# Performance work log

Measured on AMD Instinct MI355X. Metric: run time of the kernel, lower is better.

Reference implementation:

```python
import jax, jax.numpy as jnp
import numpy as np

B, S, D = 128, 200, 1024
QK = D // 8            # qk_dim_div = 8
E = 2 * D              # expand_factor = 2
RESIDUAL_DEPTH = 384.0 # repo global at model_scale=1.0
NUM_BLOCKS = 8.0
LN_EPS = 1e-5


def setup_inputs() -> dict:
    key = jax.random.key(0)
    k0, k1, k2 = jax.random.split(key, 3)
    x = jax.random.normal(k0, (B, S, D), jnp.float32)
    expand_w = (0.5 / np.sqrt(RESIDUAL_DEPTH) / 2.0) * jax.random.normal(k1, (2 * QK + 2 * E, D), jnp.float32)
    project_w = (1.0 / np.sqrt(RESIDUAL_DEPTH) / 2.0 / NUM_BLOCKS) * jax.random.normal(k2, (D, E), jnp.float32)
    ln_gamma = jnp.ones((D,), jnp.float32)
    ln_beta = jnp.zeros((D,), jnp.float32)
    position_bias_mult = jnp.asarray(1.0, jnp.float32)
    return dict(x=x, expand_w=expand_w, project_w=project_w,
                ln_gamma=ln_gamma, ln_beta=ln_beta,
                position_bias_mult=position_bias_mult)


def reference(x, expand_w, project_w, ln_gamma, ln_beta, position_bias_mult):
    _, s, d = x.shape
    qk = d // 8
    e = 2 * d
    v_dim = d

    # LayerNorm (biased variance, eps=1e-5, affine)
    mu = jnp.mean(x, axis=-1, keepdims=True)
    var = jnp.var(x, axis=-1, keepdims=True)
    xn = (x - mu) * jax.lax.rsqrt(var + LN_EPS) * ln_gamma + ln_beta

    # fused expand GEMM (dropout in eval mode = identity)
    h = jnp.einsum('bsd,ed->bse', xn, expand_w)  # [B,S,2qk+2e]
    q = h[..., :qk]
    k = h[..., qk:2 * qk]
    lin = h[..., 2 * qk:2 * qk + e]
    pre = h[..., 2 * qk + e:]

    # GEGLU: linear * exact-erf gelu
    geglu = lin * jax.nn.gelu(pre, approximate=False)
    geglu_local = geglu[..., :e - v_dim]      # [B,S,e-d]
    geglu_value = geglu[..., e - v_dim:]      # [B,S,d]

    # ALiBi-style additive causal bias: softplus(mult)*(j-i) where j<=i, -inf elsewhere
    idx = jnp.arange(s)
    causal = idx[None, :] <= idx[:, None]
    rel = (idx[None, :] - idx[:, None]).astype(x.dtype)  # j - i (<=0 on causal part)
    bias = jnp.where(causal, jax.nn.softplus(position_bias_mult) * rel,
                     jnp.asarray(-jnp.inf, x.dtype))

    # single-head SDPA, scale = 1/sqrt(qk_dim)
    scale = 1.0 / np.sqrt(qk)
    scores = jnp.einsum('bqd,bkd->bqk', q, k) * scale + bias
    attn = jax.nn.softmax(scores, axis=-1)
    att_out = jnp.einsum('bqk,bkv->bqv', attn, geglu_value)  # [B,S,d]

    out = jnp.einsum('bse,de->bsd', jnp.concatenate([geglu_local, att_out], axis=-1), project_w)
    return x + out
```

## Files before the change

kernel.cpp:

```cpp
#include <hip/hip_runtime.h>

#define B_ 128
#define S_ 200
#define D_ 1024
#define QK_ 128
#define E_ 2048
#define HE_ 4352
#define M_ (B_*S_)
#define MPAD_ (M_+32)

typedef unsigned short u16;
typedef __attribute__((ext_vector_type(8))) short bf16x8;
typedef __attribute__((ext_vector_type(4))) float fx4;
typedef __attribute__((ext_vector_type(4))) u16  usx4;

__device__ __forceinline__ u16 f2bf(float f) {
  union { float f; unsigned u; } v; v.f = f;
  unsigned r = v.u + 0x7fffu + ((v.u >> 16) & 1u);
  return (u16)(r >> 16);
}
__device__ __forceinline__ float bf2f(u16 u) {
  union { unsigned u; float f; } v; v.u = ((unsigned)u) << 16;
  return v.f;
}

__global__ __launch_bounds__(256)
void castw_kernel(const float* __restrict__ ew, const float* __restrict__ pw,
                  u16* __restrict__ ewb, u16* __restrict__ pwb) {
  const int n1 = HE_*D_/4, n2 = D_*E_/4;
  const int stride = gridDim.x * blockDim.x;
  for (int i = blockIdx.x*blockDim.x + threadIdx.x; i < n1; i += stride) {
    fx4 v = ((const fx4*)ew)[i];
    usx4 o; o[0]=f2bf(v[0]); o[1]=f2bf(v[1]); o[2]=f2bf(v[2]); o[3]=f2bf(v[3]);
    ((usx4*)ewb)[i] = o;
  }
  for (int i = blockIdx.x*blockDim.x + threadIdx.x; i < n2; i += stride) {
    fx4 v = ((const fx4*)pw)[i];
    usx4 o; o[0]=f2bf(v[0]); o[1]=f2bf(v[1]); o[2]=f2bf(v[2]); o[3]=f2bf(v[3]);
    ((usx4*)pwb)[i] = o;
  }
}

__global__ __launch_bounds__(256)
void ln_kernel(const float* __restrict__ x, const float* __restrict__ gam,
               const float* __restrict__ bet, u16* __restrict__ xn) {
  const int m = blockIdx.x, t = threadIdx.x;
  const fx4 v = *(const fx4*)(x + (size_t)m*D_ + t*4);
  float s  = v[0]+v[1]+v[2]+v[3];
  float s2 = v[0]*v[0]+v[1]*v[1]+v[2]*v[2]+v[3]*v[3];
  #pragma unroll
  for (int off = 32; off; off >>= 1) { s += __shfl_down(s, off); s2 += __shfl_down(s2, off); }
  __shared__ float red[8];
  const int l = t & 63, w = t >> 6;
  if (l == 0) { red[w] = s; red[4+w] = s2; }
  __syncthreads();
  s  = red[0]+red[1]+red[2]+red[3];
  s2 = red[4]+red[5]+red[6]+red[7];
  const float mu  = s * (1.f/D_);
  const float var = s2 * (1.f/D_) - mu*mu;
  const float rs  = rsqrtf(var + 1e-5f);
  const fx4 g4 = *(const fx4*)(gam + t*4);
  const fx4 b4 = *(const fx4*)(bet + t*4);
  usx4 o;
  #pragma unroll
  for (int j = 0; j < 4; ++j) o[j] = f2bf((v[j]-mu)*rs*g4[j] + b4[j]);
  *(usx4*)(xn + (size_t)m*D_ + t*4) = o;
}

template<int EPI>
__global__ __launch_bounds__(256)
void gemm_bt(const u16* __restrict__ A, const u16* __restrict__ Bt,
             void* __restrict__ Cp, const float* __restrict__ resid,
             int K, int ldc, int gx) {
  const int nwg = gridDim.x;
  const int q8 = nwg >> 3;
  const int swz = (blockIdx.x & 7) * q8 + (blockIdx.x >> 3);
  const int m0 = (swz / gx) * 128, n0 = (swz % gx) * 128;
  __shared__ __align__(16) u16 As[128*32];
  __shared__ __align__(16) u16 Bs[128*32];
  const int t = threadIdx.x, l = t & 63, w = t >> 6;
  const int wr = w >> 1, wc = w & 1;
  fx4 acc[4][4] = {};
  const int srow = l >> 2, scol = (l & 3) * 8;
  const u16* agp = A  + (size_t)(m0 + w*16 + srow)*K + scol;
  const u16* bgp = Bt + (size_t)(n0 + w*16 + srow)*K + scol;
  for (int k0 = 0; k0 < K; k0 += 32) {
    #pragma unroll
    for (int i = 0; i < 2; ++i) {
      __builtin_amdgcn_global_load_lds(
        (const __attribute__((address_space(1))) unsigned int*)(agp + (size_t)i*64*K + k0),
        (__attribute__((address_space(3))) unsigned int*)(As + (w*16 + i*64)*32), 16, 0, 0);
      __builtin_amdgcn_global_load_lds(
        (const __attribute__((address_space(1))) unsigned int*)(bgp + (size_t)i*64*K + k0),
        (__attribute__((address_space(3))) unsigned int*)(Bs + (w*16 + i*64)*32), 16, 0, 0);
    }
    __syncthreads();
    bf16x8 af[4], bfv[4];
    const u16* ap = As + (wr*64 + (l & 15))*32 + (l >> 4)*8;
    const u16* bp = Bs + (wc*64 + (l & 15))*32 + (l >> 4)*8;
    #pragma unroll
    for (int i = 0; i < 4; ++i) {
      af[i]  = *(const bf16x8*)(ap + i*16*32);
      bfv[i] = *(const bf16x8*)(bp + i*16*32);
    }
    #pragma unroll
    for (int mi = 0; mi < 4; ++mi)
      #pragma unroll
      for (int ni = 0; ni < 4; ++ni)
        acc[mi][ni] = __builtin_amdgcn_mfma_f32_16x16x32_bf16(af[mi], bfv[ni], acc[mi][ni], 0, 0, 0);
    __syncthreads();
  }
  const int rb = (l >> 4)*4, cb = l & 15;
  #pragma unroll
  for (int mi = 0; mi < 4; ++mi)
    #pragma unroll
    for (int ni = 0; ni < 4; ++ni) {
      const int col = n0 + wc*64 + ni*16 + cb;
      #pragma unroll
      for (int r = 0; r < 4; ++r) {
        const int row = m0 + wr*64 + mi*16 + rb + r;
        const size_t idx = (size_t)row*ldc + col;
        if (EPI == 0) ((u16*)Cp)[idx] = f2bf(acc[mi][ni][r]);
        else          ((float*)Cp)[idx] = acc[mi][ni][r] + resid[idx];
      }
    }
}

__global__ __launch_bounds__(256)
void fused_expand(const u16* __restrict__ A, const u16* __restrict__ Bt,
                  u16* __restrict__ A2, float* __restrict__ Vv) {
  const int nwg = gridDim.x;
  const int q8 = nwg >> 3;
  const int swz = (blockIdx.x & 7) * q8 + (blockIdx.x >> 3);
  const int m0 = (swz >> 4) * 128;
  const int n0e = (swz & 15) * 128;
  __shared__ __align__(16) u16 As[128*32];
  __shared__ __align__(16) u16 Bs[128*32];
  const int t = threadIdx.x, l = t & 63, w = t >> 6;
  const int wr = w >> 1, wc = w & 1;
  const int srow = l >> 2, scol = (l & 3) * 8;
  const u16* agp = A + (size_t)(m0 + w*16 + srow)*D_ + scol;
  const u16* bgp_pre = Bt + (size_t)(2*QK_ + E_ + n0e + w*16 + srow)*D_ + scol;
  const u16* bgp_lin = Bt + (size_t)(2*QK_ + n0e + w*16 + srow)*D_ + scol;
  fx4 acc[4][4];
  unsigned gp[4][4][2];
  #pragma unroll
  for (int pass = 0; pass < 2; ++pass) {
    const u16* bgp = pass ? bgp_lin : bgp_pre;
    #pragma unroll
    for (int mi = 0; mi < 4; ++mi)
      #pragma unroll
      for (int ni = 0; ni < 4; ++ni) acc[mi][ni] = (fx4){0.f,0.f,0.f,0.f};
    for (int k0 = 0; k0 < D_; k0 += 32) {
      #pragma unroll
      for (int i = 0; i < 2; ++i) {
        __builtin_amdgcn_global_load_lds(
          (const __attribute__((address_space(1))) unsigned int*)(agp + (size_t)i*64*D_ + k0),
          (__attribute__((address_space(3))) unsigned int*)(As + (w*16 + i*64)*32), 16, 0, 0);
        __builtin_amdgcn_global_load_lds(
          (const __attribute__((address_space(1))) unsigned int*)(bgp + (size_t)i*64*D_ + k0),
          (__attribute__((address_space(3))) unsigned int*)(Bs + (w*16 + i*64)*32), 16, 0, 0);
      }
      __syncthreads();
      bf16x8 af[4], bfv[4];
      const u16* ap = As + (wr*64 + (l & 15))*32 + (l >> 4)*8;
      const u16* bp = Bs + (wc*64 + (l & 15))*32 + (l >> 4)*8;
      #pragma unroll
      for (int i = 0; i < 4; ++i) {
        af[i]  = *(const bf16x8*)(ap + i*16*32);
        bfv[i] = *(const bf16x8*)(bp + i*16*32);
      }
      #pragma unroll
      for (int mi = 0; mi < 4; ++mi)
        #pragma unroll
        for (int ni = 0; ni < 4; ++ni)
          acc[mi][ni] = __builtin_amdgcn_mfma_f32_16x16x32_bf16(af[mi], bfv[ni], acc[mi][ni], 0, 0, 0);
      __syncthreads();
    }
    if (pass == 0) {
      #pragma unroll
      for (int mi = 0; mi < 4; ++mi)
        #pragma unroll
        for (int ni = 0; ni < 4; ++ni)
          #pragma unroll
          for (int h = 0; h < 2; ++h) {
            float p0 = acc[mi][ni][2*h],   g0 = 0.5f*p0*(1.f + erff(p0*0.70710678f));
            float p1 = acc[mi][ni][2*h+1], g1 = 0.5f*p1*(1.f + erff(p1*0.70710678f));
            gp[mi][ni][h] = (unsigned)f2bf(g0) | ((unsigned)f2bf(g1) << 16);
          }
    }
  }
  const int rb = (l >> 4)*4, cb = l & 15;
  #pragma unroll
  for (int mi = 0; mi < 4; ++mi)
    #pragma unroll
    for (int ni = 0; ni < 4; ++ni) {
      const int colc = wc*64 + ni*16 + cb;
      #pragma unroll
      for (int r = 0; r < 4; ++r) {
        const int row = m0 + wr*64 + mi*16 + rb + r;
        const float gv = bf2f((u16)(gp[mi][ni][r>>1] >> ((r&1)*16)));
        const float v = acc[mi][ni][r] * gv;
        if (n0e < D_) A2[(size_t)row*E_ + n0e + colc] = f2bf(v);
        else          Vv[(size_t)row*D_ + (n0e - D_) + colc] = v;
      }
    }
}

__global__ __launch_bounds__(256)
void attn_kernel(const u16* __restrict__ QKb, const float* __restrict__ Vv,
                 const float* __restrict__ pbm, u16* __restrict__ A2) {
  const int b = blockIdx.y, qt = blockIdx.x;
  const int qbase = qt*32;
  const int kmax = (S_ < qbase+32) ? S_ : qbase+32;
  const int nkt = (kmax + 15) >> 4;
  const int t = threadIdx.x, l = t & 63, w = t >> 6;
  __shared__ float ScT[208][40];
  float sp; { float p = pbm[0]; sp = (p > 20.f) ? p : log1pf(__expf(p)); }
  const float scale = 0.08838834764831845f;

  const int ntiles = 2*nkt;
  for (int tile = w; tile < ntiles; tile += 4) {
    const int qt16 = tile & 1, kt16 = tile >> 1;
    const int q0 = qbase + qt16*16, k0 = kt16*16;
    if (k0 > q0 + 15) continue;
    fx4 acc = {0.f, 0.f, 0.f, 0.f};
    const u16* qp = QKb + (size_t)(b*S_ + q0 + (l & 15))*256 + (l >> 4)*8;
    const u16* kp = QKb + (size_t)(b*S_ + k0 + (l & 15))*256 + QK_ + (l >> 4)*8;
    #pragma unroll
    for (int ks = 0; ks < 4; ++ks) {
      bf16x8 a  = *(const bf16x8*)(qp + ks*32);
      bf16x8 bb = *(const bf16x8*)(kp + ks*32);
      acc = __builtin_amdgcn_mfma_f32_16x16x32_bf16(a, bb, acc, 0, 0, 0);
    }
    const int kcol = k0 + (l & 15);
    #pragma unroll
    for (int r = 0; r < 4; ++r) {
      const int qg = q0 + (l >> 4)*4 + r;
      float s = acc[r]*scale + sp*(float)(kcol - qg);
      if (kcol > qg || qg >= S_ || kcol >= S_) s = -1e30f;
      ScT[kcol][qt16*16 + (l >> 4)*4 + r] = s;
    }
  }
  __syncthreads();
  {
    const int r = t >> 3, j = t & 7;
    const int qg = qbase + r;
    if (qg < S_) {
      float mx = -1e30f;
      for (int k = j; k <= qg; k += 8) mx = fmaxf(mx, ScT[k][r]);
      #pragma unroll
      for (int msk = 1; msk < 8; msk <<= 1) mx = fmaxf(mx, __shfl_xor(mx, msk));
      float sum = 0.f;
      for (int k = j; k <= qg; k += 8) { float p = __expf(ScT[k][r] - mx); ScT[k][r] = p; sum += p; }
      #pragma unroll
      for (int msk = 1; msk < 8; msk <<= 1) sum += __shfl_xor(sum, msk);
      const float inv = 1.f / sum;
      for (int k = j; k <= qg; k += 8) ScT[k][r] *= inv;
      for (int k = qg+1+j; k < kmax; k += 8) ScT[k][r] = 0.f;
    }
  }
  __syncthreads();
  fx4 acc[32];
  #pragma unroll
  for (int i = 0; i < 32; ++i) acc[i] = (fx4){0.f,0.f,0.f,0.f};
  const float* vb = Vv + (size_t)b*S_*D_ + w*256 + l*4;
  for (int k = 0; k < kmax; ++k) {
    const fx4 v4 = *(const fx4*)(vb + (size_t)k*D_);
    #pragma unroll
    for (int g = 0; g < 8; ++g) {
      const fx4 p4 = *(const fx4*)&ScT[k][g*4];
      #pragma unroll
      for (int j = 0; j < 4; ++j) acc[g*4+j] += v4 * p4[j];
    }
  }
  #pragma unroll
  for (int qi = 0; qi < 32; ++qi) {
    const int qg = qbase + qi;
    if (qg < S_) {
      usx4 o;
      #pragma unroll
      for (int j = 0; j < 4; ++j) o[j] = f2bf(acc[qi][j]);
      *(usx4*)(A2 + (size_t)(b*S_ + qg)*E_ + D_ + w*256 + l*4) = o;
    }
  }
}

extern "C" void kernel_launch(void* const* d_in, const int* in_sizes, int n_in,
                              void* d_out, int out_size, void* d_ws, size_t ws_size,
                              hipStream_t stream) {
  (void)in_sizes; (void)n_in; (void)out_size; (void)ws_size;
  const float* x   = (const float*)d_in[0];
  const float* ew  = (const float*)d_in[1];
  const float* pw  = (const float*)d_in[2];
  const float* gam = (const float*)d_in[3];
  const float* bet = (const float*)d_in[4];
  const float* pbm = (const float*)d_in[5];
  float* out = (float*)d_out;

  char* ws = (char*)d_ws;
  size_t off = 0;
  auto alloc = [&](size_t bytes) -> void* {
    void* p = ws + off; off += (bytes + 255) & ~(size_t)255; return p;
  };
  u16* xn  = (u16*)alloc((size_t)M_   * D_  * 2);
  u16* QKb = (u16*)alloc((size_t)MPAD_* 256 * 2);
  u16* A2  = (u16*)alloc((size_t)M_   * E_  * 2);
  u16* ewb = (u16*)alloc((size_t)HE_  * D_  * 2);
  u16* pwb = (u16*)alloc((size_t)D_   * E_  * 2);
  float* Vv = out;

  castw_kernel<<<1024, 256, 0, stream>>>(ew, pw, ewb, pwb);
  ln_kernel<<<M_, 256, 0, stream>>>(x, gam, bet, xn);
  gemm_bt<0><<<(256/128)*(M_/128), 256, 0, stream>>>(xn, ewb, QKb, nullptr, D_, 256, 256/128);
  fused_expand<<<(E_/128)*(M_/128), 256, 0, stream>>>(xn, ewb, A2, Vv);
  attn_kernel<<<dim3((S_+31)/32, B_), 256, 0, stream>>>(QKb, Vv, pbm, A2);
  gemm_bt<1><<<(D_/128)*(M_/128), 256, 0, stream>>>(A2, pwb, out, x, E_, D_, D_/128);
}
```

Before: 1.183 ms.

## Double-buffer GEMM LDS tiles and fuse expand pre/lin passes into one K loop

Both GEMM kernels now double-buffer their LDS tiles. The next K-slice is issued with global_load_lds before the current one is computed, using explicit vmcnt waits and barriers so loads overlap with the MFMA work. The fused expand kernel no longer runs two sequential K passes (gelu pre, then lin). It accumulates both in one loop that shares the A tile, which halves A-tile loads. The cost is double the accumulator registers and three times the LDS, which can lower occupancy or cause spills.

```diff
diff --git a/kernel.cpp b/kernel.cpp
--- a/kernel.cpp
+++ b/kernel.cpp
@@ -23,6 +23,11 @@
   union { unsigned u; float f; } v; v.u = ((unsigned)u) << 16;
   return v.f;
 }
+
+#define GLOAD(gptr, lptr) \
+  __builtin_amdgcn_global_load_lds( \
+      (const __attribute__((address_space(1))) unsigned int*)(gptr), \
+      (__attribute__((address_space(3))) unsigned int*)(lptr), 16, 0, 0)
 
 __global__ __launch_bounds__(256)
 void castw_kernel(const float* __restrict__ ew, const float* __restrict__ pw,
@@ -76,40 +81,59 @@
   const int q8 = nwg >> 3;
   const int swz = (blockIdx.x & 7) * q8 + (blockIdx.x >> 3);
   const int m0 = (swz / gx) * 128, n0 = (swz % gx) * 128;
-  __shared__ __align__(16) u16 As[128*32];
-  __shared__ __align__(16) u16 Bs[128*32];
+  __shared__ __align__(16) u16 As[2][128*32];
+  __shared__ __align__(16) u16 Bs[2][128*32];
   const int t = threadIdx.x, l = t & 63, w = t >> 6;
   const int wr = w >> 1, wc = w & 1;
   fx4 acc[4][4] = {};
   const int srow = l >> 2, scol = (l & 3) * 8;
   const u16* agp = A  + (size_t)(m0 + w*16 + srow)*K + scol;
   const u16* bgp = Bt + (size_t)(n0 + w*16 + srow)*K + scol;
-  for (int k0 = 0; k0 < K; k0 += 32) {
-    #pragma unroll
-    for (int i = 0; i < 2; ++i) {
-      __builtin_amdgcn_global_load_lds(
-        (const __attribute__((address_space(1))) unsigned int*)(agp + (size_t)i*64*K + k0),
-        (__attribute__((address_space(3))) unsigned int*)(As + (w*16 + i*64)*32), 16, 0, 0);
-      __builtin_amdgcn_global_load_lds(
-        (const __attribute__((address_space(1))) unsigned int*)(bgp + (size_t)i*64*K + k0),
-        (__attribute__((address_space(3))) unsigned int*)(Bs + (w*16 + i*64)*32), 16, 0, 0);
-    }
-    __syncthreads();
-    bf16x8 af[4], bfv[4];
-    const u16* ap = As + (wr*64 + (l & 15))*32 + (l >> 4)*8;
-    const u16* bp = Bs + (wc*64 + (l & 15))*32 + (l >> 4)*8;
-    #pragma unroll
-    for (int i = 0; i < 4; ++i) {
-      af[i]  = *(const bf16x8*)(ap + i*16*32);
-      bfv[i] = *(const bf16x8*)(bp + i*16*32);
-    }
-    #pragma unroll
-    for (int mi = 0; mi < 4; ++mi)
-      #pragma unroll
-      for (int ni = 0; ni < 4; ++ni)
-        acc[mi][ni] = __builtin_amdgcn_mfma_f32_16x16x32_bf16(af[mi], bfv[ni], acc[mi][ni], 0, 0, 0);
-    __syncthreads();
-  }
+  const int loff = (w*16 + srow)*32 + scol;
+
+  #define STAGE_G(bi, k0) do { \
+    GLOAD(agp + (k0),            &As[bi][loff]); \
+    GLOAD(agp + 64*K + (k0),     &As[bi][loff + 64*32]); \
+    GLOAD(bgp + (k0),            &Bs[bi][loff]); \
+    GLOAD(bgp + 64*K + (k0),     &Bs[bi][loff + 64*32]); \
+  } while (0)
+
+  #define COMPUTE_G(bi) do { \
+    bf16x8 af[4], bfv[4]; \
+    const u16* ap = &As[bi][(wr*64 + (l & 15))*32 + (l >> 4)*8]; \
+    const u16* bp = &Bs[bi][(wc*64 + (l & 15))*32 + (l >> 4)*8]; \
+    _Pragma("unroll") \
+    for (int i = 0; i < 4; ++i) { \
+      af[i]  = *(const bf16x8*)(ap + i*16*32); \
+      bfv[i] = *(const bf16x8*)(bp + i*16*32); \
+    } \
+    _Pragma("unroll") \
+    for (int mi = 0; mi < 4; ++mi) \
+      _Pragma("unroll") \
+      for (int ni = 0; ni < 4; ++ni) \
+        acc[mi][ni] = __builtin_amdgcn_mfma_f32_16x16x32_bf16(af[mi], bfv[ni], acc[mi][ni], 0, 0, 0); \
+  } while (0)
+
+  const int NT = K >> 5;
+  STAGE_G(0, 0);
+  int cur = 0;
+  for (int kt = 0; kt < NT-1; ++kt) {
+    STAGE_G(cur^1, (kt+1)*32);
+    asm volatile("s_waitcnt vmcnt(4)" ::: "memory");
+    __builtin_amdgcn_s_barrier();
+    asm volatile("" ::: "memory");
+    COMPUTE_G(cur);
+    asm volatile("" ::: "memory");
+    __builtin_amdgcn_s_barrier();
+    cur ^= 1;
+  }
+  asm volatile("s_waitcnt vmcnt(0)" ::: "memory");
+  __builtin_amdgcn_s_barrier();
+  asm volatile("" ::: "memory");
+  COMPUTE_G(cur);
+  #undef STAGE_G
+  #undef COMPUTE_G
+
   const int rb = (l >> 4)*4, cb = l & 15;
   #pragma unroll
   for (int mi = 0; mi < 4; ++mi)
@@ -134,62 +158,68 @@
   const int swz = (blockIdx.x & 7) * q8 + (blockIdx.x >> 3);
   const int m0 = (swz >> 4) * 128;
   const int n0e = (swz & 15) * 128;
-  __shared__ __align__(16) u16 As[128*32];
-  __shared__ __align__(16) u16 Bs[128*32];
+  __shared__ __align__(16) u16 As[2][128*32];
+  __shared__ __align__(16) u16 Bps[2][128*32];
+  __shared__ __align__(16) u16 Bls[2][128*32];
   const int t = threadIdx.x, l = t & 63, w = t >> 6;
   const int wr = w >> 1, wc = w & 1;
   const int srow = l >> 2, scol = (l & 3) * 8;
   const u16* agp = A + (size_t)(m0 + w*16 + srow)*D_ + scol;
   const u16* bgp_pre = Bt + (size_t)(2*QK_ + E_ + n0e + w*16 + srow)*D_ + scol;
   const u16* bgp_lin = Bt + (size_t)(2*QK_ + n0e + w*16 + srow)*D_ + scol;
-  fx4 acc[4][4];
-  unsigned gp[4][4][2];
-  #pragma unroll
-  for (int pass = 0; pass < 2; ++pass) {
-    const u16* bgp = pass ? bgp_lin : bgp_pre;
-    #pragma unroll
-    for (int mi = 0; mi < 4; ++mi)
-      #pragma unroll
-      for (int ni = 0; ni < 4; ++ni) acc[mi][ni] = (fx4){0.f,0.f,0.f,0.f};
-    for (int k0 = 0; k0 < D_; k0 += 32) {
-      #pragma unroll
-      for (int i = 0; i < 2; ++i) {
-        __builtin_amdgcn_global_load_lds(
-          (const __attribute__((address_space(1))) unsigned int*)(agp + (size_t)i*64*D_ + k0),
-          (__attribute__((address_space(3))) unsigned int*)(As + (w*16 + i*64)*32), 16, 0, 0);
-        __builtin_amdgcn_global_load_lds(
-          (const __attribute__((address_space(1))) unsigned int*)(bgp + (size_t)i*64*D_ + k0),
-          (__attribute__((address_space(3))) unsigned int*)(Bs + (w*16 + i*64)*32), 16, 0, 0);
-      }
-      __syncthreads();
-      bf16x8 af[4], bfv[4];
-      const u16* ap = As + (wr*64 + (l & 15))*32 + (l >> 4)*8;
-      const u16* bp = Bs + (wc*64 + (l & 15))*32 + (l >> 4)*8;
-      #pragma unroll
-      for (int i = 0; i < 4; ++i) {
-        af[i]  = *(const bf16x8*)(ap + i*16*32);
-        bfv[i] = *(const bf16x8*)(bp + i*16*32);
-      }
-      #pragma unroll
-      for (int mi = 0; mi < 4; ++mi)
-        #pragma unroll
-        for (int ni = 0; ni < 4; ++ni)
-          acc[mi][ni] = __builtin_amdgcn_mfma_f32_16x16x32_bf16(af[mi], bfv[ni], acc[mi][ni], 0, 0, 0);
-      __syncthreads();
-    }
-    if (pass == 0) {
-      #pragma unroll
-      for (int mi = 0; mi < 4; ++mi)
-        #pragma unroll
-        for (int ni = 0; ni < 4; ++ni)
-          #pragma unroll
-          for (int h = 0; h < 2; ++h) {
-            float p0 = acc[mi][ni][2*h],   g0 = 0.5f*p0*(1.f + erff(p0*0.70710678f));
-            float p1 = acc[mi][ni][2*h+1], g1 = 0.5f*p1*(1.f + erff(p1*0.70710678f));
-            gp[mi][ni][h] = (unsigned)f2bf(g0) | ((unsigned)f2bf(g1) << 16);
-          }
-    }
-  }
+  const int loff = (w*16 + srow)*32 + scol;
+  fx4 accp[4][4] = {};
+  fx4 accl[4][4] = {};
+
+  #define STAGE_F(bi, k0) do { \
+    GLOAD(agp + (k0),               &As[bi][loff]); \
+    GLOAD(agp + 64*D_ + (k0),       &As[bi][loff + 64*32]); \
+    GLOAD(bgp_pre + (k0),           &Bps[bi][loff]); \
+    GLOAD(bgp_pre + 64*D_ + (k0),   &Bps[bi][loff + 64*32]); \
+    GLOAD(bgp_lin + (k0),           &Bls[bi][loff]); \
+    GLOAD(bgp_lin + 64*D_ + (k0),   &Bls[bi][loff + 64*32]); \
+  } while (0)
+
+  #define COMPUTE_F(bi) do { \
+    bf16x8 af[4], bfp[4], bfl[4]; \
+    const u16* ap  = &As[bi][(wr*64 + (l & 15))*32 + (l >> 4)*8]; \
+    const u16* bpp = &Bps[bi][(wc*64 + (l & 15))*32 + (l >> 4)*8]; \
+    const u16* bpl = &Bls[bi][(wc*64 + (l & 15))*32 + (l >> 4)*8]; \
+    _Pragma("unroll") \
+    for (int i = 0; i < 4; ++i) { \
+      af[i]  = *(const bf16x8*)(ap  + i*16*32); \
+      bfp[i] = *(const bf16x8*)(bpp + i*16*32); \
+      bfl[i] = *(const bf16x8*)(bpl + i*16*32); \
+    } \
+    _Pragma("unroll") \
+    for (int mi = 0; mi < 4; ++mi) \
+      _Pragma("unroll") \
+      for (int ni = 0; ni < 4; ++ni) { \
+        accp[mi][ni] = __builtin_amdgcn_mfma_f32_16x16x32_bf16(af[mi], bfp[ni], accp[mi][ni], 0, 0, 0); \
+        accl[mi][ni] = __builtin_amdgcn_mfma_f32_16x16x32_bf16(af[mi], bfl[ni], accl[mi][ni], 0, 0, 0); \
+      } \
+  } while (0)
+
+  const int NT = D_ >> 5;
+  STAGE_F(0, 0);
+  int cur = 0;
+  for (int kt = 0; kt < NT-1; ++kt) {
+    STAGE_F(cur^1, (kt+1)*32);
+    asm volatile("s_waitcnt vmcnt(6)" ::: "memory");
+    __builtin_amdgcn_s_barrier();
+    asm volatile("" ::: "memory");
+    COMPUTE_F(cur);
+    asm volatile("" ::: "memory");
+    __builtin_amdgcn_s_barrier();
+    cur ^= 1;
+  }
+  asm volatile("s_waitcnt vmcnt(0)" ::: "memory");
+  __builtin_amdgcn_s_barrier();
+  asm volatile("" ::: "memory");
+  COMPUTE_F(cur);
+  #undef STAGE_F
+  #undef COMPUTE_F
+
   const int rb = (l >> 4)*4, cb = l & 15;
   #pragma unroll
   for (int mi = 0; mi < 4; ++mi)
@@ -199,8 +229,9 @@
       #pragma unroll
       for (int r = 0; r < 4; ++r) {
         const int row = m0 + wr*64 + mi*16 + rb + r;
-        const float gv = bf2f((u16)(gp[mi][ni][r>>1] >> ((r&1)*16)));
-        const float v = acc[mi][ni][r] * gv;
+        const float p = accp[mi][ni][r];
+        const float g = 0.5f*p*(1.f + erff(p*0.70710678f));
+        const float v = accl[mi][ni][r] * g;
         if (n0e < D_) A2[(size_t)row*E_ + n0e + colc] = f2bf(v);
         else          Vv[(size_t)row*D_ + (n0e - D_) + colc] = v;
       }
```

Result: faster. 950.6 us (-19.6%).
